# Optimization experiments

Measured on AMD Instinct MI355X. Metric: run time of the kernel, lower is better.

## Reference

```python
import itertools
import jax, jax.numpy as jnp
import numpy as np

GRID_SIZE = (8, 8)
B, C, T, M = 16, 306, 4096, 270


def setup_inputs() -> dict:
    key = jax.random.key(0)
    kx, kp, kw = jax.random.split(key, 3)
    x = jax.random.normal(kx, (B, C, T), dtype=jnp.float32)
    # positions in [-1, 0.74] keeps ceil index < grid_size (the original torch
    # code goes out of bounds for positions at/near +1)
    positions = jax.random.uniform(kp, (B, C, 2), dtype=jnp.float32,
                                   minval=-1.0, maxval=0.74)
    grid_weights = jax.random.normal(kw, (M, int(np.prod(GRID_SIZE))), dtype=jnp.float32)
    return {"x": x, "positions": positions, "grid_weights": grid_weights}


def reference(x, positions, grid_weights):
    # x: [B, C, T], positions: [B, C, D], grid_weights: [M, G]
    gs = jnp.asarray(GRID_SIZE, dtype=x.dtype)
    D = len(GRID_SIZE)
    G = int(np.prod(GRID_SIZE))
    strides = [int(np.prod(GRID_SIZE[d + 1:])) for d in range(D)]

    grid_pos = (positions + 1.0) * gs / 2.0       # [B, C, D] in [0, grid_size)
    low = jnp.floor(grid_pos)
    idx_low = low.astype(jnp.int32)               # [B, C, D]
    idx_high = jnp.ceil(grid_pos).astype(jnp.int32)
    w_high = grid_pos - low                       # fractional part
    w_low = 1.0 - w_high

    b_idx = jnp.arange(x.shape[0])[:, None]       # [B, 1] batch index for scatter
    grid_values = jnp.zeros((x.shape[0], G, x.shape[2]), dtype=x.dtype)

    # 2^D = 4 corners: multilinear interpolation scatter-add into flat grid
    for combo in itertools.product((0, 1), repeat=D):
        idx = jnp.zeros(idx_low.shape[:-1], dtype=jnp.int32)
        w = jnp.ones(w_low.shape[:-1], dtype=x.dtype)
        for d, hi in enumerate(combo):
            idx = idx + (idx_high if hi else idx_low)[..., d] * strides[d]
            w = w * (w_high if hi else w_low)[..., d]
        grid_values = grid_values.at[b_idx, idx].add(x * w[..., None])

    # [M, G] x [B, G, T] -> [B, M, T]
    return jnp.einsum('mg,bgt->bmt', grid_weights, grid_values)
```

## Files before the change

### kernel.cpp

```cpp
#include <hip/hip_runtime.h>
#include <cstdint>

#define B_   16
#define C_   306
#define T_   4096
#define M_   270
#define G_   64
#define MT_  17
#define KB_  10
#define TT   64
#define BDIM 256
#define NW   4

typedef __attribute__((ext_vector_type(8))) short s8;
typedef __attribute__((ext_vector_type(4))) float f4;
typedef __attribute__((ext_vector_type(4))) int   i4;

__device__ __forceinline__ short f2bf(float f) {
    unsigned u = __builtin_bit_cast(unsigned, f);
    u += 0x7FFFu + ((u >> 16) & 1u);
    return (short)(u >> 16);
}
__device__ __forceinline__ float bf2f(short h) {
    return __builtin_bit_cast(float, ((unsigned)(unsigned short)h) << 16);
}

__global__ __launch_bounds__(BDIM) void a_build(const float* __restrict__ pos,
                                                const float* __restrict__ gw,
                                                i4* __restrict__ Ah,
                                                i4* __restrict__ Al) {
    __shared__ float At[16][321];
    const int mt  = blockIdx.x;
    const int b   = blockIdx.y;
    const int tid = threadIdx.x;
    const int mr  = tid & 15;
    const int cg  = tid >> 4;
    const int m   = mt * 16 + mr;

    for (int c = cg; c < KB_ * 32; c += 16) {
        float v = 0.0f;
        if (c < C_ && m < M_) {
            const float* pp = pos + ((size_t)b * C_ + c) * 2;
            float gp0 = (pp[0] + 1.0f) * 4.0f;
            float gp1 = (pp[1] + 1.0f) * 4.0f;
            float f0 = floorf(gp0), f1 = floorf(gp1);
            int l0 = (int)f0, l1 = (int)f1;
            int h0 = (int)ceilf(gp0), h1 = (int)ceilf(gp1);
            float wh0 = gp0 - f0, wh1 = gp1 - f1;
            float wl0 = 1.0f - wh0, wl1 = 1.0f - wh1;
            const float* wm = gw + (size_t)m * G_;
            v = wl0 * wl1 * wm[l0 * 8 + l1] + wl0 * wh1 * wm[l0 * 8 + h1]
              + wh0 * wl1 * wm[h0 * 8 + l1] + wh0 * wh1 * wm[h0 * 8 + h1];
        }
        At[mr][c] = v;
    }
    __syncthreads();

    const int lane = tid & 63;
    const int mr2  = lane & 15;
    const int j0   = (lane >> 4) * 8;
    for (int kb = tid >> 6; kb < KB_; kb += 4) {
        s8 hv, lv;
        #pragma unroll
        for (int j = 0; j < 8; ++j) {
            float v = At[mr2][kb * 32 + j0 + j];
            short h = f2bf(v);
            hv[j] = h;
            lv[j] = f2bf(v - bf2f(h));
        }
        const int idx = ((b * MT_ + mt) * KB_ + kb) * 64 + lane;
        Ah[idx] = __builtin_bit_cast(i4, hv);
        Al[idx] = __builtin_bit_cast(i4, lv);
    }
}

__global__ __launch_bounds__(BDIM, 3) void gemm_kernel(
    const float* __restrict__ x, const i4* __restrict__ Ahp,
    const i4* __restrict__ Alp, float* __restrict__ out) {
    __shared__ s8 BhT[2][320];
    __shared__ s8 BlT[2][320];

    const int b    = blockIdx.y;
    const int t0   = blockIdx.x * TT;
    const int tid  = threadIdx.x;
    const int lane = tid & 63;
    const int wave = __builtin_amdgcn_readfirstlane(tid >> 6);
    const int quad = lane >> 4;
    const int lcol = lane & 15;
    const int col  = tid & 63;
    const int rp   = (tid >> 6) * 2;

    const float* xrow = x + (size_t)b * C_ * T_ + t0 + col;

    float r0[4], r1[4];
    #pragma unroll
    for (int i = 0; i < 4; ++i) {
        const int c0 = rp + 8 * i;
        r0[i] = xrow[(size_t)c0 * T_];
        r1[i] = xrow[(size_t)(c0 + 1) * T_];
    }
    {
        unsigned* wh = (unsigned*)&BhT[0][0];
        unsigned* wl = (unsigned*)&BlT[0][0];
        #pragma unroll
        for (int i = 0; i < 4; ++i) {
            short h0 = f2bf(r0[i]), h1 = f2bf(r1[i]);
            short l0 = f2bf(r0[i] - bf2f(h0)), l1 = f2bf(r1[i] - bf2f(h1));
            wh[col * 20 + (rp >> 1) + 4 * i] =
                (unsigned)(unsigned short)h0 | ((unsigned)(unsigned short)h1 << 16);
            wl[col * 20 + (rp >> 1) + 4 * i] =
                (unsigned)(unsigned short)l0 | ((unsigned)(unsigned short)l1 << 16);
        }
    }
    __syncthreads();

    f4 acc[5][4];
    #pragma unroll
    for (int mi = 0; mi < 5; ++mi)
        #pragma unroll
        for (int nt = 0; nt < 4; ++nt)
            acc[mi][nt] = (f4){0.f, 0.f, 0.f, 0.f};

    int cur = 0;
    for (int kb = 0; kb < KB_; ++kb) {
        const int  nxt = cur ^ 1;
        const bool pf  = (kb + 1 < KB_);

        if (pf) {
            #pragma unroll
            for (int i = 0; i < 4; ++i) {
                const int c0 = (kb + 1) * 32 + rp + 8 * i;
                r0[i] = (c0 < C_)     ? xrow[(size_t)c0 * T_]       : 0.0f;
                r1[i] = (c0 + 1 < C_) ? xrow[(size_t)(c0 + 1) * T_] : 0.0f;
            }
        }

        s8 bh[4], bl[4];
        #pragma unroll
        for (int nt = 0; nt < 4; ++nt) {
            bh[nt] = BhT[cur][(nt * 16 + lcol) * 5 + quad];
            bl[nt] = BlT[cur][(nt * 16 + lcol) * 5 + quad];
        }

        #pragma unroll
        for (int mi = 0; mi < 5; ++mi) {
            const int mt = wave + mi * NW;
            if (mt < MT_) {
                const int idx = ((b * MT_ + mt) * KB_ + kb) * 64 + lane;
                const s8 ah = __builtin_bit_cast(s8, Ahp[idx]);
                const s8 al = __builtin_bit_cast(s8, Alp[idx]);
                #pragma unroll
                for (int nt = 0; nt < 4; ++nt) {
                    f4 a = acc[mi][nt];
                    a = __builtin_amdgcn_mfma_f32_16x16x32_bf16(al, bh[nt], a, 0, 0, 0);
                    a = __builtin_amdgcn_mfma_f32_16x16x32_bf16(ah, bl[nt], a, 0, 0, 0);
                    a = __builtin_amdgcn_mfma_f32_16x16x32_bf16(ah, bh[nt], a, 0, 0, 0);
                    acc[mi][nt] = a;
                }
            }
        }

        if (pf) {
            unsigned* wh = (unsigned*)&BhT[nxt][0];
            unsigned* wl = (unsigned*)&BlT[nxt][0];
            #pragma unroll
            for (int i = 0; i < 4; ++i) {
                short h0 = f2bf(r0[i]), h1 = f2bf(r1[i]);
                short l0 = f2bf(r0[i] - bf2f(h0)), l1 = f2bf(r1[i] - bf2f(h1));
                wh[col * 20 + (rp >> 1) + 4 * i] =
                    (unsigned)(unsigned short)h0 | ((unsigned)(unsigned short)h1 << 16);
                wl[col * 20 + (rp >> 1) + 4 * i] =
                    (unsigned)(unsigned short)l0 | ((unsigned)(unsigned short)l1 << 16);
            }
        }
        __syncthreads();
        cur = nxt;
    }

    float* op = out + (size_t)b * M_ * T_ + t0;
    #pragma unroll
    for (int mi = 0; mi < 5; ++mi) {
        const int mt = wave + mi * NW;
        if (mt < MT_) {
            const int mrow = mt * 16 + quad * 4;
            #pragma unroll
            for (int nt = 0; nt < 4; ++nt) {
                #pragma unroll
                for (int r = 0; r < 4; ++r) {
                    const int m = mrow + r;
                    if (m < M_)
                        op[(size_t)m * T_ + nt * 16 + lcol] = acc[mi][nt][r];
                }
            }
        }
    }
}

extern "C" void kernel_launch(void* const* d_in, const int* in_sizes, int n_in,
                              void* d_out, int out_size, void* d_ws, size_t ws_size,
                              hipStream_t stream) {
    const float* x   = (const float*)d_in[0];
    const float* pos = (const float*)d_in[1];
    const float* gw  = (const float*)d_in[2];
    float* out = (float*)d_out;

    i4* Ah = (i4*)d_ws;
    i4* Al = (i4*)((char*)d_ws + 2785280);

    a_build<<<dim3(MT_, B_), BDIM, 0, stream>>>(pos, gw, Ah, Al);

    dim3 grid(T_ / TT, B_);
    gemm_kernel<<<grid, BDIM, 0, stream>>>(x, Ah, Al, out);
}
```

Measured before the change: 213.7 us.

## Prefetch A fragments into registers and write B tiles as 16-byte vectors

The GEMM kernel now loads the A hi/lo fragments for the next K block into a register double buffer, so global loads overlap the current block's MFMAs. Each thread loads 8 consecutive channels of x and writes one 16-byte s8 vector per tile into LDS instead of several packed 32-bit writes. The K loop is fully unrolled and launch bounds drop from 3 to 2 waves per SIMD. This frees registers for the extra buffers but lowers occupancy.

```diff
diff --git a/kernel.cpp b/kernel.cpp
--- a/kernel.cpp
+++ b/kernel.cpp
@@ -74,7 +74,7 @@
     }
 }
 
-__global__ __launch_bounds__(BDIM, 3) void gemm_kernel(
+__global__ __launch_bounds__(BDIM, 2) void gemm_kernel(
     const float* __restrict__ x, const i4* __restrict__ Ahp,
     const i4* __restrict__ Alp, float* __restrict__ out) {
     __shared__ s8 BhT[2][320];
@@ -88,31 +88,36 @@
     const int quad = lane >> 4;
     const int lcol = lane & 15;
     const int col  = tid & 63;
-    const int rp   = (tid >> 6) * 2;
 
     const float* xrow = x + (size_t)b * C_ * T_ + t0 + col;
-
-    float r0[4], r1[4];
-    #pragma unroll
-    for (int i = 0; i < 4; ++i) {
-        const int c0 = rp + 8 * i;
-        r0[i] = xrow[(size_t)c0 * T_];
-        r1[i] = xrow[(size_t)(c0 + 1) * T_];
-    }
+    const i4* Abase_h = Ahp + (size_t)(b * MT_ * KB_) * 64 + lane;
+    const i4* Abase_l = Alp + (size_t)(b * MT_ * KB_) * 64 + lane;
+
+    float rv[8];
+    #pragma unroll
+    for (int j = 0; j < 8; ++j)
+        rv[j] = xrow[(size_t)(8 * wave + j) * T_];
     {
-        unsigned* wh = (unsigned*)&BhT[0][0];
-        unsigned* wl = (unsigned*)&BlT[0][0];
-        #pragma unroll
-        for (int i = 0; i < 4; ++i) {
-            short h0 = f2bf(r0[i]), h1 = f2bf(r1[i]);
-            short l0 = f2bf(r0[i] - bf2f(h0)), l1 = f2bf(r1[i] - bf2f(h1));
-            wh[col * 20 + (rp >> 1) + 4 * i] =
-                (unsigned)(unsigned short)h0 | ((unsigned)(unsigned short)h1 << 16);
-            wl[col * 20 + (rp >> 1) + 4 * i] =
-                (unsigned)(unsigned short)l0 | ((unsigned)(unsigned short)l1 << 16);
-        }
-    }
-    __syncthreads();
+        s8 hv, lv;
+        #pragma unroll
+        for (int j = 0; j < 8; ++j) {
+            short h = f2bf(rv[j]);
+            hv[j] = h;
+            lv[j] = f2bf(rv[j] - bf2f(h));
+        }
+        BhT[0][col * 5 + wave] = hv;
+        BlT[0][col * 5 + wave] = lv;
+    }
+
+    s8 ah[2][5], al[2][5];
+    #pragma unroll
+    for (int mi = 0; mi < 5; ++mi) {
+        const int mt = wave + mi * NW;
+        if (mt < MT_) {
+            ah[0][mi] = __builtin_bit_cast(s8, Abase_h[(mt * KB_) * 64]);
+            al[0][mi] = __builtin_bit_cast(s8, Abase_l[(mt * KB_) * 64]);
+        }
+    }
 
     f4 acc[5][4];
     #pragma unroll
@@ -121,17 +126,31 @@
         for (int nt = 0; nt < 4; ++nt)
             acc[mi][nt] = (f4){0.f, 0.f, 0.f, 0.f};
 
-    int cur = 0;
+    __syncthreads();
+
+    #pragma unroll
     for (int kb = 0; kb < KB_; ++kb) {
+        const int  cur = kb & 1;
         const int  nxt = cur ^ 1;
         const bool pf  = (kb + 1 < KB_);
 
         if (pf) {
             #pragma unroll
-            for (int i = 0; i < 4; ++i) {
-                const int c0 = (kb + 1) * 32 + rp + 8 * i;
-                r0[i] = (c0 < C_)     ? xrow[(size_t)c0 * T_]       : 0.0f;
-                r1[i] = (c0 + 1 < C_) ? xrow[(size_t)(c0 + 1) * T_] : 0.0f;
+            for (int j = 0; j < 8; ++j) {
+                const int c0 = (kb + 1) * 32 + 8 * wave + j;
+                rv[j] = (c0 < C_) ? xrow[(size_t)c0 * T_] : 0.0f;
+            }
+        }
+
+        if (pf) {
+            #pragma unroll
+            for (int mi = 0; mi < 5; ++mi) {
+                const int mt = wave + mi * NW;
+                if (mt < MT_) {
+                    const int idx = (mt * KB_ + kb + 1) * 64;
+                    ah[nxt][mi] = __builtin_bit_cast(s8, Abase_h[idx]);
+                    al[nxt][mi] = __builtin_bit_cast(s8, Abase_l[idx]);
+                }
             }
         }
 
@@ -146,35 +165,29 @@
         for (int mi = 0; mi < 5; ++mi) {
             const int mt = wave + mi * NW;
             if (mt < MT_) {
-                const int idx = ((b * MT_ + mt) * KB_ + kb) * 64 + lane;
-                const s8 ah = __builtin_bit_cast(s8, Ahp[idx]);
-                const s8 al = __builtin_bit_cast(s8, Alp[idx]);
                 #pragma unroll
                 for (int nt = 0; nt < 4; ++nt) {
                     f4 a = acc[mi][nt];
-                    a = __builtin_amdgcn_mfma_f32_16x16x32_bf16(al, bh[nt], a, 0, 0, 0);
-                    a = __builtin_amdgcn_mfma_f32_16x16x32_bf16(ah, bl[nt], a, 0, 0, 0);
-                    a = __builtin_amdgcn_mfma_f32_16x16x32_bf16(ah, bh[nt], a, 0, 0, 0);
+                    a = __builtin_amdgcn_mfma_f32_16x16x32_bf16(al[cur][mi], bh[nt], a, 0, 0, 0);
+                    a = __builtin_amdgcn_mfma_f32_16x16x32_bf16(ah[cur][mi], bl[nt], a, 0, 0, 0);
+                    a = __builtin_amdgcn_mfma_f32_16x16x32_bf16(ah[cur][mi], bh[nt], a, 0, 0, 0);
                     acc[mi][nt] = a;
                 }
             }
         }
 
         if (pf) {
-            unsigned* wh = (unsigned*)&BhT[nxt][0];
-            unsigned* wl = (unsigned*)&BlT[nxt][0];
-            #pragma unroll
-            for (int i = 0; i < 4; ++i) {
-                short h0 = f2bf(r0[i]), h1 = f2bf(r1[i]);
-                short l0 = f2bf(r0[i] - bf2f(h0)), l1 = f2bf(r1[i] - bf2f(h1));
-                wh[col * 20 + (rp >> 1) + 4 * i] =
-                    (unsigned)(unsigned short)h0 | ((unsigned)(unsigned short)h1 << 16);
-                wl[col * 20 + (rp >> 1) + 4 * i] =
-                    (unsigned)(unsigned short)l0 | ((unsigned)(unsigned short)l1 << 16);
-            }
+            s8 hv, lv;
+            #pragma unroll
+            for (int j = 0; j < 8; ++j) {
+                short h = f2bf(rv[j]);
+                hv[j] = h;
+                lv[j] = f2bf(rv[j] - bf2f(h));
+            }
+            BhT[nxt][col * 5 + wave] = hv;
+            BlT[nxt][col * 5 + wave] = lv;
         }
         __syncthreads();
-        cur = nxt;
     }
 
     float* op = out + (size_t)b * M_ * T_ + t0;
```

New measurement: 185.1 us. 13.4% less time.
